# Kernel optimization log

Hardware: AMD Instinct MI355X
Metric: run time of the kernel (lower is better)

## Reference

```python
import jax, jax.numpy as jnp
import numpy as np

P = 16            # decode steps == n_process
M = 4             # number of physical nodes
CAPACITY = [4, 4, 4, 4]
B = 4096          # batch
S = 16            # n_process (sequence length)
G = 128           # gnn_dim
E = 256           # n_embed
H = 512           # n_hidden
CLIP = 10.0       # clip_logits
MASK_PENALTY = 1e8


def setup_inputs() -> dict:
    key = jax.random.key(0)
    ks = jax.random.split(key, 16)
    u = lambda k, shape: jax.random.uniform(k, shape, jnp.float32, -0.08, 0.08)
    return {
        "x": jax.random.normal(ks[0], (B, S, G), jnp.float32),
        "emb_W": u(ks[1], (E, G)),                 # embedding Linear (no bias)
        "enc_Wih": u(ks[2], (4 * H, E)),           # encoder LSTM (gate order i,f,g,o)
        "enc_Whh": u(ks[3], (4 * H, H)),
        "enc_b": u(ks[4], (4 * H,)),               # b_ih + b_hh folded into one bias
        "dec_Wih": u(ks[5], (4 * H, E)),           # decoder LSTM
        "dec_Whh": u(ks[6], (4 * H, H)),
        "dec_b": u(ks[7], (4 * H,)),
        "Wq2": u(ks[8], (H, H)),                   # pointer W_q2
        "bq2": u(ks[9], (H,)),
        "Wref2": u(ks[10], (H, H)),                # pointer W_ref2 (conv1d k=1 == linear)
        "bref2": u(ks[11], (H,)),
        "Vec2": u(ks[12], (H,)),
        "dec_input0": u(ks[13], (E,)),             # learned initial decoder input
    }


def lstm_cell(x, h, c, Wih, Whh, b):
    g = x @ Wih.T + h @ Whh.T + b
    i, f, gg, o = jnp.split(g, 4, axis=-1)
    c = jax.nn.sigmoid(f) * c + jax.nn.sigmoid(i) * jnp.tanh(gg)
    h = jax.nn.sigmoid(o) * jnp.tanh(c)
    return h, c


def reference(x, emb_W, enc_Wih, enc_Whh, enc_b, dec_Wih, dec_Whh, dec_b,
              Wq2, bq2, Wref2, bref2, Vec2, dec_input0):
    Bx, Sx, _ = x.shape
    emb = x @ emb_W.T                                  # (B,S,E)

    # ---- encoder LSTM over the sequence ----
    def enc_step(carry, xt):
        h, c = carry
        h, c = lstm_cell(xt, h, c, enc_Wih, enc_Whh, enc_b)
        return (h, c), h

    h0 = jnp.zeros((Bx, H), emb.dtype)
    (h, c), enc_hs = jax.lax.scan(enc_step, (h0, h0), jnp.swapaxes(emb, 0, 1))
    ref = jnp.swapaxes(enc_hs, 0, 1)                   # (B,S,H)

    # W_ref2 conv1d(k=1) applied to ref is step-invariant: hoist out of the loop
    u2 = jnp.einsum('bsh,oh->bso', ref, Wref2) + bref2  # (B,S,H)

    dec0 = jnp.broadcast_to(dec_input0, (Bx, E))
    mask0 = jnp.zeros((Bx, Sx), emb.dtype)

    def dec_step(carry, _):
        h, c, din, mask = carry
        h, c = lstm_cell(din, h, c, dec_Wih, dec_Whh, dec_b)
        qp = h @ Wq2.T + bq2                           # (B,H)
        t = CLIP * jnp.tanh(qp[:, None, :] + u2)       # (B,S,H)
        logits = jnp.einsum('h,bsh->bs', Vec2, t) - MASK_PENALTY * mask
        log_p = jax.nn.log_softmax(logits, axis=-1)    # (B,S)
        nxt = jnp.argmax(log_p, axis=1)                # greedy node selector
        din = jnp.take_along_axis(emb, nxt[:, None, None], axis=1)[:, 0, :]
        mask = mask + jax.nn.one_hot(nxt, Sx, dtype=mask.dtype)
        return (h, c, din, mask), (nxt, log_p)

    _, (pis, log_ps) = jax.lax.scan(dec_step, (h, c, dec0, mask0), None, length=P)
    pi = jnp.swapaxes(pis, 0, 1)                       # (B,P)
    log_ps = jnp.swapaxes(log_ps, 0, 1)                # (B,P,S)

    # log-likelihood of the chosen tour
    ll = jnp.take_along_axis(log_ps, pi[:, :, None], axis=2)[..., 0].sum(axis=1)

    # __get_mapping: node id per step depends only on the capacity vector
    nodes = jnp.asarray(np.repeat(np.arange(M), np.asarray(CAPACITY))[:P], jnp.int32)
    rows = jnp.arange(Bx)
    mapping = jnp.full((Bx, P), -1, jnp.int32)
    mapping = mapping.at[rows[:, None], pi].set(jnp.broadcast_to(nodes, (Bx, P)))
    return mapping, ll
```

## Files before the change

### kernel.cpp

```cpp
#include <hip/hip_runtime.h>
#include <cstddef>

#define Bsz  4096
#define Sseq 16
#define Gdim 128
#define Edim 256
#define Hdim 512
#define H4   2048
#define Psteps 16
#define BK   16

typedef short bfrag8 __attribute__((ext_vector_type(8)));
typedef float f32x4  __attribute__((ext_vector_type(4)));

__device__ __forceinline__ void split3(float f, unsigned short& h,
                                       unsigned short& m, unsigned short& l) {
    unsigned u = __float_as_uint(f);
    h = (unsigned short)(u >> 16);
    float r1 = f - __uint_as_float(u & 0xffff0000u);
    unsigned u1 = __float_as_uint(r1);
    m = (unsigned short)(u1 >> 16);
    float r2 = r1 - __uint_as_float(u1 & 0xffff0000u);
    l = (unsigned short)(__float_as_uint(r2) >> 16);
}

__global__ void fold_kernel(const float* __restrict__ encWih,
                            const float* __restrict__ encWhh,
                            const float* __restrict__ enc_b,
                            const float* __restrict__ decWih,
                            const float* __restrict__ decWhh,
                            const float* __restrict__ dec_b,
                            const float* __restrict__ embW,
                            const float* __restrict__ dec0,
                            unsigned short* __restrict__ encEh,
                            unsigned short* __restrict__ encEm,
                            unsigned short* __restrict__ encEl,
                            unsigned short* __restrict__ encWh,
                            unsigned short* __restrict__ encWm,
                            unsigned short* __restrict__ encWl,
                            unsigned short* __restrict__ decEh,
                            unsigned short* __restrict__ decEm,
                            unsigned short* __restrict__ decEl,
                            unsigned short* __restrict__ decWh,
                            unsigned short* __restrict__ decWm,
                            unsigned short* __restrict__ decWl,
                            float* __restrict__ encBI, float* __restrict__ decBI,
                            float* __restrict__ v0bI) {
    const int o = blockIdx.x;
    const int gate = o >> 9, j = o & 511;
    const int c = j * 4 + gate;
    const int g = threadIdx.x;
    float se = 0.f, sd = 0.f;
    for (int e = 0; e < Edim; ++e) {
        float w = embW[e * Gdim + g];
        se += encWih[(size_t)o * Edim + e] * w;
        sd += decWih[(size_t)o * Edim + e] * w;
    }
    unsigned short h, m, l;
    split3(se, h, m, l);
    encEh[(size_t)c * Gdim + g] = h; encEm[(size_t)c * Gdim + g] = m;
    encEl[(size_t)c * Gdim + g] = l;
    split3(sd, h, m, l);
    decEh[(size_t)c * Gdim + g] = h; decEm[(size_t)c * Gdim + g] = m;
    decEl[(size_t)c * Gdim + g] = l;
    for (int k = g; k < Hdim; k += Gdim) {
        split3(encWhh[(size_t)o * Hdim + k], h, m, l);
        encWh[(size_t)c * Hdim + k] = h; encWm[(size_t)c * Hdim + k] = m;
        encWl[(size_t)c * Hdim + k] = l;
        split3(decWhh[(size_t)o * Hdim + k], h, m, l);
        decWh[(size_t)c * Hdim + k] = h; decWm[(size_t)c * Hdim + k] = m;
        decWl[(size_t)c * Hdim + k] = l;
    }
    if (g == 0) {
        encBI[c] = enc_b[o];
        decBI[c] = dec_b[o];
        float s = dec_b[o];
        for (int e = 0; e < Edim; ++e) s += decWih[(size_t)o * Edim + e] * dec0[e];
        v0bI[c] = s;
    }
}

__global__ __launch_bounds__(256) void gates_mfma(
    const unsigned short* __restrict__ Wh1, const unsigned short* __restrict__ Wm1,
    const unsigned short* __restrict__ Wl1, int K1,
    const float* __restrict__ X, int ldx,
    const int* __restrict__ gather, int gmul,
    const unsigned short* __restrict__ Wh2, const unsigned short* __restrict__ Wm2,
    const unsigned short* __restrict__ Wl2, int K2,
    const float* __restrict__ Hin,
    const float* __restrict__ biasI,
    const float* __restrict__ c_in, float* __restrict__ h_out,
    float* __restrict__ c_out, int czero)
{
    __shared__ __align__(16) unsigned short wlds[2][3 * 4096];
    __shared__ __align__(16) float alds[2][128 * 32];

    const int tid = threadIdx.x;
    const int wv = tid >> 6, lane = tid & 63;
    const int lm = lane & 15, quad = lane >> 4;
    const int c0 = blockIdx.y * 128;
    const int mB0 = blockIdx.x * 128;

    int mrow[2];
#pragma unroll
    for (int tm = 0; tm < 2; ++tm) mrow[tm] = mB0 + wv * 32 + tm * 16 + lm;

    int srow[2], sqs[2];
#pragma unroll
    for (int i = 0; i < 2; ++i) {
        const int seg = i * 4 + wv;
        const int r = seg * 16 + (lane >> 2);
        srow[i] = r;
        sqs[i] = (lane & 3) ^ ((r >> 1) & 3);
    }
    size_t roff1[2], roff2[2];
#pragma unroll
    for (int i = 0; i < 2; ++i) {
        roff1[i] = (size_t)(c0 + srow[i]) * K1 + (size_t)(sqs[i] * 8);
        roff2[i] = (size_t)(c0 + srow[i]) * K2 + (size_t)(sqs[i] * 8);
    }

    const int asw = ((lane & 7) ^ (lane >> 3)) * 4;
    const float* asrcX[4];
    const float* asrcH[4];
#pragma unroll
    for (int i = 0; i < 4; ++i) {
        const int r = (wv * 4 + i) * 8 + (lane >> 3);
        const int m = mB0 + r;
        if (X) {
            size_t off = (size_t)m * ldx;
            if (gather) off += (size_t)gather[m] * gmul;
            asrcX[i] = X + off + asw;
        }
        if (Hin) asrcH[i] = Hin + (size_t)m * K2 + asw;
    }

    int boffW[8];
#pragma unroll
    for (int tn = 0; tn < 8; ++tn) {
        const int r = tn * 16 + lm;
        boffW[tn] = r * 32 + ((quad ^ ((r >> 1) & 3)) * 8);
    }
    int boffA1[2], boffA2[2];
#pragma unroll
    for (int tm = 0; tm < 2; ++tm) {
        const int r = wv * 32 + tm * 16 + lm;
        boffA1[tm] = r * 32 + (((2 * quad)     ^ (lm & 7)) << 2);
        boffA2[tm] = r * 32 + (((2 * quad + 1) ^ (lm & 7)) << 2);
    }

    auto stage = [&](int kcN, int buf) {
        const bool nX = kcN < K1;
        const int kb = nX ? kcN : kcN - K1;
#pragma unroll
        for (int i = 0; i < 2; ++i) {
            const int seg = i * 4 + wv;
            unsigned short* lb = &wlds[buf][seg * 512];
            const unsigned short* gh = (nX ? Wh1 + roff1[i] : Wh2 + roff2[i]) + kb;
            const unsigned short* gm = (nX ? Wm1 + roff1[i] : Wm2 + roff2[i]) + kb;
            const unsigned short* gl = (nX ? Wl1 + roff1[i] : Wl2 + roff2[i]) + kb;
            __builtin_amdgcn_global_load_lds(
                (const __attribute__((address_space(1))) void*)gh,
                (__attribute__((address_space(3))) void*)(lb), 16, 0, 0);
            __builtin_amdgcn_global_load_lds(
                (const __attribute__((address_space(1))) void*)gm,
                (__attribute__((address_space(3))) void*)(lb + 4096), 16, 0, 0);
            __builtin_amdgcn_global_load_lds(
                (const __attribute__((address_space(1))) void*)gl,
                (__attribute__((address_space(3))) void*)(lb + 8192), 16, 0, 0);
        }
#pragma unroll
        for (int i = 0; i < 4; ++i) {
            float* lb = &alds[buf][(wv * 4 + i) * 256];
            const float* src = (nX ? asrcX[i] : asrcH[i]) + kb;
            __builtin_amdgcn_global_load_lds(
                (const __attribute__((address_space(1))) void*)src,
                (__attribute__((address_space(3))) void*)lb, 16, 0, 0);
        }
    };

    f32x4 acc[8][2];
#pragma unroll
    for (int i = 0; i < 8; ++i)
#pragma unroll
        for (int j = 0; j < 2; ++j) acc[i][j] = (f32x4){0.f, 0.f, 0.f, 0.f};

    const int KT = K1 + K2;
    stage(0, 0);
    int cur = 0;

    for (int kc = 0; kc < KT; kc += 32) {
        __syncthreads();
        if (kc + 32 < KT) stage(kc + 32, cur ^ 1);

        const float* abuf = alds[cur];
        bfrag8 bh[2], bm[2], bl[2];
#pragma unroll
        for (int tm = 0; tm < 2; ++tm) {
            float a8[8];
            *(float4*)&a8[0] = *(const float4*)(abuf + boffA1[tm]);
            *(float4*)&a8[4] = *(const float4*)(abuf + boffA2[tm]);
#pragma unroll
            for (int j = 0; j < 8; ++j) {
                unsigned short h, m, l;
                split3(a8[j], h, m, l);
                bh[tm][j] = (short)h; bm[tm][j] = (short)m; bl[tm][j] = (short)l;
            }
        }

        const unsigned short* bufp = wlds[cur];
#pragma unroll
        for (int hh = 0; hh < 2; ++hh) {
            bfrag8 ah[4], am4[4], al[4];
#pragma unroll
            for (int t = 0; t < 4; ++t) {
                const int tn = hh * 4 + t;
                ah[t]  = *(const bfrag8*)(bufp + boffW[tn]);
                am4[t] = *(const bfrag8*)(bufp + 4096 + boffW[tn]);
                al[t]  = *(const bfrag8*)(bufp + 8192 + boffW[tn]);
            }
#pragma unroll
            for (int tm = 0; tm < 2; ++tm) {
#pragma unroll
                for (int t = 0; t < 4; ++t) {
                    const int tn = hh * 4 + t;
                    f32x4 c = acc[tn][tm];
                    c = __builtin_amdgcn_mfma_f32_16x16x32_bf16(ah[t], bl[tm], c, 0, 0, 0);
                    c = __builtin_amdgcn_mfma_f32_16x16x32_bf16(al[t], bh[tm], c, 0, 0, 0);
                    c = __builtin_amdgcn_mfma_f32_16x16x32_bf16(am4[t], bm[tm], c, 0, 0, 0);
                    c = __builtin_amdgcn_mfma_f32_16x16x32_bf16(ah[t], bm[tm], c, 0, 0, 0);
                    c = __builtin_amdgcn_mfma_f32_16x16x32_bf16(am4[t], bh[tm], c, 0, 0, 0);
                    c = __builtin_amdgcn_mfma_f32_16x16x32_bf16(ah[t], bh[tm], c, 0, 0, 0);
                    acc[tn][tm] = c;
                }
            }
        }
        cur ^= 1;
    }

#pragma unroll
    for (int tn = 0; tn < 8; ++tn) {
        const int nb = c0 + tn * 16 + quad * 4;
        float4 bb = *(const float4*)(biasI + nb);
        const int j = nb >> 2;
#pragma unroll
        for (int tm = 0; tm < 2; ++tm) {
            const size_t idx = (size_t)mrow[tm] * Hdim + j;
            float gi = acc[tn][tm][0] + bb.x;
            float gf = acc[tn][tm][1] + bb.y;
            float gg = acc[tn][tm][2] + bb.z;
            float go = acc[tn][tm][3] + bb.w;
            float si = 1.f / (1.f + expf(-gi));
            float sf = 1.f / (1.f + expf(-gf));
            float so = 1.f / (1.f + expf(-go));
            float co = czero ? 0.f : c_in[idx];
            float cn = si * tanhf(gg) + sf * co;
            c_out[idx] = cn;
            h_out[idx] = so * tanhf(cn);
        }
    }
}

__global__ __launch_bounds__(256, 4) void gemm_sm(const float* __restrict__ A,
                                                  const float* __restrict__ W,
                                                  const float* __restrict__ bias,
                                                  float* __restrict__ C, int ldc)
{
    __shared__ float As[BK][64];
    __shared__ float Bs[BK][64];
    const int tid = threadIdx.x;
    const int rowBase = blockIdx.y * 64;
    const int colBase = blockIdx.x * 64;
    const int wv = tid >> 6;
    const int waveX = wv & 1, waveY = wv >> 1;
    const int lane = tid & 63;
    const int lx = lane & 7, ly = lane >> 3;
    const int rOff = waveY * 32 + ly * 4;
    const int cOff = waveX * 32 + lx * 4;

    const int ra = tid & 63;
    const int ka = (tid >> 6) * 4;
    const float* arow = A + (size_t)(rowBase + ra) * Hdim + ka;
    const float* brow = W + (size_t)(colBase + ra) * Hdim + ka;

    float4 aR, bR;
    float acc[4][4];
#pragma unroll
    for (int i = 0; i < 4; ++i)
#pragma unroll
        for (int j = 0; j < 4; ++j) acc[i][j] = 0.f;

    aR = *(const float4*)(arow);
    bR = *(const float4*)(brow);
    for (int kt = 0; kt < Hdim; kt += BK) {
        __syncthreads();
        As[ka + 0][ra] = aR.x; As[ka + 1][ra] = aR.y;
        As[ka + 2][ra] = aR.z; As[ka + 3][ra] = aR.w;
        Bs[ka + 0][ra] = bR.x; Bs[ka + 1][ra] = bR.y;
        Bs[ka + 2][ra] = bR.z; Bs[ka + 3][ra] = bR.w;
        __syncthreads();
        if (kt + BK < Hdim) {
            aR = *(const float4*)(arow + kt + BK);
            bR = *(const float4*)(brow + kt + BK);
        }
#pragma unroll
        for (int kk = 0; kk < BK; ++kk) {
            float4 av = *(const float4*)&As[kk][rOff];
            float4 bv = *(const float4*)&Bs[kk][cOff];
            const float* ap = (const float*)&av;
            const float* bp = (const float*)&bv;
#pragma unroll
            for (int i = 0; i < 4; ++i)
#pragma unroll
                for (int j = 0; j < 4; ++j) acc[i][j] += ap[i] * bp[j];
        }
    }

    float4 bb = *(const float4*)(bias + colBase + cOff);
#pragma unroll
    for (int i = 0; i < 4; ++i) {
        const int row = rowBase + rOff + i;
        float4 o;
        o.x = acc[i][0] + bb.x;
        o.y = acc[i][1] + bb.y;
        o.z = acc[i][2] + bb.z;
        o.w = acc[i][3] + bb.w;
        *(float4*)(C + (size_t)row * ldc + colBase + cOff) = o;
    }
}

__global__ __launch_bounds__(256) void attn_step(const float* __restrict__ qp,
                                                 const float* __restrict__ u2,
                                                 const float* __restrict__ Vec2,
                                                 float* __restrict__ mask,
                                                 float* __restrict__ ll_ws,
                                                 int* __restrict__ nxt,
                                                 float* __restrict__ out_map,
                                                 float* __restrict__ out_ll,
                                                 int step, int node) {
    const int b = blockIdx.x;
    __shared__ float qpS[Hdim];
    __shared__ float vS[Hdim];
    __shared__ float logitS[Sseq];
    const int tid = threadIdx.x;
    qpS[tid]       = qp[(size_t)b * Hdim + tid];
    qpS[tid + 256] = qp[(size_t)b * Hdim + 256 + tid];
    vS[tid]        = Vec2[tid];
    vS[tid + 256]  = Vec2[256 + tid];
    __syncthreads();

    const int wave = tid >> 6, lane = tid & 63;
    for (int si = 0; si < 4; ++si) {
        int s = wave * 4 + si;
        const float* u2p = u2 + ((size_t)b * Sseq + s) * Hdim;
        float sum = 0.f;
#pragma unroll
        for (int i = 0; i < 8; ++i) {
            int hh = lane + i * 64;
            sum += vS[hh] * tanhf(qpS[hh] + u2p[hh]);
        }
        for (int off = 32; off > 0; off >>= 1) sum += __shfl_down(sum, off);
        if (lane == 0) {
            float pen = step ? mask[b * Sseq + s] * 1e8f : 0.f;
            logitS[s] = 10.f * sum - pen;
        }
    }
    __syncthreads();

    if (tid == 0) {
        float mx = logitS[0];
        int am = 0;
        for (int s = 1; s < Sseq; ++s)
            if (logitS[s] > mx) { mx = logitS[s]; am = s; }
        float se = 0.f;
        for (int s = 0; s < Sseq; ++s) se += expf(logitS[s] - mx);
        float lp = -logf(se);
        float llv = (step ? ll_ws[b] : 0.f) + lp;
        ll_ws[b] = llv;
        out_ll[b] = llv;
        nxt[b] = am;
        if (step == 0) {
            for (int s = 0; s < Sseq; ++s) mask[b * Sseq + s] = (s == am) ? 1.f : 0.f;
        } else {
            mask[b * Sseq + am] += 1.f;
        }
        out_map[b * Sseq + am] = (float)node;
    }
}

extern "C" void kernel_launch(void* const* d_in, const int* in_sizes, int n_in,
                              void* d_out, int out_size, void* d_ws, size_t ws_size,
                              hipStream_t stream) {
    const float* x       = (const float*)d_in[0];
    const float* emb_W   = (const float*)d_in[1];
    const float* enc_Wih = (const float*)d_in[2];
    const float* enc_Whh = (const float*)d_in[3];
    const float* enc_b   = (const float*)d_in[4];
    const float* dec_Wih = (const float*)d_in[5];
    const float* dec_Whh = (const float*)d_in[6];
    const float* dec_b   = (const float*)d_in[7];
    const float* Wq2     = (const float*)d_in[8];
    const float* bq2     = (const float*)d_in[9];
    const float* Wref2   = (const float*)d_in[10];
    const float* bref2   = (const float*)d_in[11];
    const float* Vec2    = (const float*)d_in[12];
    const float* dec0    = (const float*)d_in[13];

    float* ws      = (float*)d_ws;
    float* u2      = ws;
    float* h0      = u2 + (size_t)Bsz * Sseq * Hdim;
    float* c0      = h0 + (size_t)Bsz * Hdim;
    float* h1      = c0 + (size_t)Bsz * Hdim;
    float* c1      = h1 + (size_t)Bsz * Hdim;
    float* qp      = c1 + (size_t)Bsz * Hdim;
    float* mask    = qp + (size_t)Bsz * Hdim;
    float* ll      = mask + (size_t)Bsz * Sseq;
    int*   nxt     = (int*)(ll + Bsz);
    float* encBI   = (float*)(nxt + Bsz);
    float* decBI   = encBI + H4;
    float* v0bI    = decBI + H4;
    unsigned short* us = (unsigned short*)(v0bI + H4);
    unsigned short* encEh = us;                       us += (size_t)H4 * Gdim;
    unsigned short* encEm = us;                       us += (size_t)H4 * Gdim;
    unsigned short* encEl = us;                       us += (size_t)H4 * Gdim;
    unsigned short* encWh = us;                       us += (size_t)H4 * Hdim;
    unsigned short* encWm = us;                       us += (size_t)H4 * Hdim;
    unsigned short* encWl = us;                       us += (size_t)H4 * Hdim;
    unsigned short* decEh = us;                       us += (size_t)H4 * Gdim;
    unsigned short* decEm = us;                       us += (size_t)H4 * Gdim;
    unsigned short* decEl = us;                       us += (size_t)H4 * Gdim;
    unsigned short* decWh = us;                       us += (size_t)H4 * Hdim;
    unsigned short* decWm = us;                       us += (size_t)H4 * Hdim;
    unsigned short* decWl = us;                       us += (size_t)H4 * Hdim;

    float* out_map = (float*)d_out;
    float* out_ll  = out_map + (size_t)Bsz * Psteps;

    static const int nodes[Psteps] = {0,0,0,0, 1,1,1,1, 2,2,2,2, 3,3,3,3};

    fold_kernel<<<H4, Gdim, 0, stream>>>(enc_Wih, enc_Whh, enc_b,
                                         dec_Wih, dec_Whh, dec_b,
                                         emb_W, dec0,
                                         encEh, encEm, encEl, encWh, encWm, encWl,
                                         decEh, decEm, decEl, decWh, decWm, decWl,
                                         encBI, decBI, v0bI);

    const dim3 gBig(32, 16);
    const dim3 gSm(8, 64);

    for (int t = 0; t < Sseq; ++t) {
        float* ho = (t & 1) ? h0 : h1;
        float* co = (t & 1) ? c0 : c1;
        const float* hi = (t & 1) ? h1 : h0;
        const float* ci = (t & 1) ? c1 : c0;
        if (t == 0) {
            gates_mfma<<<gBig, 256, 0, stream>>>(
                encEh, encEm, encEl, Gdim,
                x, Sseq * Gdim, nullptr, 0,
                nullptr, nullptr, nullptr, 0, nullptr,
                encBI, ci, ho, co, 1);
        } else {
            gates_mfma<<<gBig, 256, 0, stream>>>(
                encEh, encEm, encEl, Gdim,
                x + t * Gdim, Sseq * Gdim, nullptr, 0,
                encWh, encWm, encWl, Hdim, hi,
                encBI, ci, ho, co, 0);
        }
        gemm_sm<<<gSm, 256, 0, stream>>>(ho, Wref2, bref2,
                                         u2 + (size_t)t * Hdim, Sseq * Hdim);
    }

    for (int p = 0; p < Psteps; ++p) {
        const int u = Sseq + p;
        float* ho = (u & 1) ? h0 : h1;
        float* co = (u & 1) ? c0 : c1;
        const float* hi = (u & 1) ? h1 : h0;
        const float* ci = (u & 1) ? c1 : c0;
        if (p == 0) {
            gates_mfma<<<gBig, 256, 0, stream>>>(
                nullptr, nullptr, nullptr, 0,
                nullptr, 0, nullptr, 0,
                decWh, decWm, decWl, Hdim, hi,
                v0bI, ci, ho, co, 0);
        } else {
            gates_mfma<<<gBig, 256, 0, stream>>>(
                decEh, decEm, decEl, Gdim,
                x, Sseq * Gdim, nxt, Gdim,
                decWh, decWm, decWl, Hdim, hi,
                decBI, ci, ho, co, 0);
        }
        gemm_sm<<<gSm, 256, 0, stream>>>(ho, Wq2, bq2, qp, Hdim);
        attn_step<<<Bsz, 256, 0, stream>>>(qp, u2, Vec2, mask, ll, nxt,
                                           out_map, out_ll, p, nodes[p]);
    }
}
```

Baseline: 3.862 ms.

## Replace FP32 SIMT projection GEMMs with split-bf16 MFMA kernels

The W_ref2 and W_q2 projections, run once per encoder and decoder step, move from a scalar FP32 tiled GEMM to an MFMA kernel. It splits weights and activations into three bf16 parts and runs six cross-product MFMAs to keep close to FP32 accuracy. Weights are pre-split once by a new fold kernel and staged into LDS with double-buffered direct global-to-LDS loads and swizzled layouts. The fold kernel also caches the Wih rows in shared memory instead of re-reading them from global memory. The cost is extra workspace, a small one-time setup pass, and accuracy that depends on the three-way split.

Result: faster. 3.252 ms (-15.8%).

```diff
diff --git a/kernel.cpp b/kernel.cpp
--- a/kernel.cpp
+++ b/kernel.cpp
@@ -46,15 +46,23 @@
                             unsigned short* __restrict__ decWl,
                             float* __restrict__ encBI, float* __restrict__ decBI,
                             float* __restrict__ v0bI) {
+    __shared__ float rE[Edim], rD[Edim];
     const int o = blockIdx.x;
     const int gate = o >> 9, j = o & 511;
     const int c = j * 4 + gate;
     const int g = threadIdx.x;
+    rE[g]        = encWih[(size_t)o * Edim + g];
+    rE[g + Gdim] = encWih[(size_t)o * Edim + g + Gdim];
+    rD[g]        = decWih[(size_t)o * Edim + g];
+    rD[g + Gdim] = decWih[(size_t)o * Edim + g + Gdim];
+    __syncthreads();
+
     float se = 0.f, sd = 0.f;
+#pragma unroll 8
     for (int e = 0; e < Edim; ++e) {
         float w = embW[e * Gdim + g];
-        se += encWih[(size_t)o * Edim + e] * w;
-        sd += decWih[(size_t)o * Edim + e] * w;
+        se += rE[e] * w;
+        sd += rD[e] * w;
     }
     unsigned short h, m, l;
     split3(se, h, m, l);
@@ -75,8 +83,28 @@
         encBI[c] = enc_b[o];
         decBI[c] = dec_b[o];
         float s = dec_b[o];
-        for (int e = 0; e < Edim; ++e) s += decWih[(size_t)o * Edim + e] * dec0[e];
+        for (int e = 0; e < Edim; ++e) s += rD[e] * dec0[e];
         v0bI[c] = s;
+    }
+}
+
+__global__ __launch_bounds__(256) void fold_proj(
+    const float* __restrict__ Wr, const float* __restrict__ Wq,
+    unsigned short* __restrict__ rWh, unsigned short* __restrict__ rWm,
+    unsigned short* __restrict__ rWl,
+    unsigned short* __restrict__ qWh, unsigned short* __restrict__ qWm,
+    unsigned short* __restrict__ qWl) {
+    const int o = blockIdx.x;
+    const float* src = blockIdx.y ? Wq : Wr;
+    unsigned short* ph = blockIdx.y ? qWh : rWh;
+    unsigned short* pm = blockIdx.y ? qWm : rWm;
+    unsigned short* pl = blockIdx.y ? qWl : rWl;
+    for (int k = threadIdx.x; k < Hdim; k += 256) {
+        unsigned short h, m, l;
+        split3(src[(size_t)o * Hdim + k], h, m, l);
+        ph[(size_t)o * Hdim + k] = h;
+        pm[(size_t)o * Hdim + k] = m;
+        pl[(size_t)o * Hdim + k] = l;
     }
 }
 
@@ -261,71 +289,116 @@
     }
 }
 
-__global__ __launch_bounds__(256, 4) void gemm_sm(const float* __restrict__ A,
-                                                  const float* __restrict__ W,
-                                                  const float* __restrict__ bias,
-                                                  float* __restrict__ C, int ldc)
+__global__ __launch_bounds__(256) void proj_mfma(
+    const unsigned short* __restrict__ Wh, const unsigned short* __restrict__ Wm,
+    const unsigned short* __restrict__ Wl,
+    const float* __restrict__ A,
+    const float* __restrict__ bias,
+    float* __restrict__ C, int ldc)
 {
-    __shared__ float As[BK][64];
-    __shared__ float Bs[BK][64];
+    __shared__ __align__(16) unsigned short wlds[2][3 * 2048];
+    __shared__ __align__(16) float alds[2][64 * 32];
+
     const int tid = threadIdx.x;
-    const int rowBase = blockIdx.y * 64;
-    const int colBase = blockIdx.x * 64;
-    const int wv = tid >> 6;
-    const int waveX = wv & 1, waveY = wv >> 1;
-    const int lane = tid & 63;
-    const int lx = lane & 7, ly = lane >> 3;
-    const int rOff = waveY * 32 + ly * 4;
-    const int cOff = waveX * 32 + lx * 4;
-
-    const int ra = tid & 63;
-    const int ka = (tid >> 6) * 4;
-    const float* arow = A + (size_t)(rowBase + ra) * Hdim + ka;
-    const float* brow = W + (size_t)(colBase + ra) * Hdim + ka;
-
-    float4 aR, bR;
-    float acc[4][4];
-#pragma unroll
-    for (int i = 0; i < 4; ++i)
-#pragma unroll
-        for (int j = 0; j < 4; ++j) acc[i][j] = 0.f;
-
-    aR = *(const float4*)(arow);
-    bR = *(const float4*)(brow);
-    for (int kt = 0; kt < Hdim; kt += BK) {
+    const int wv = tid >> 6, lane = tid & 63;
+    const int lm = lane & 15, quad = lane >> 4;
+    const int nB0 = blockIdx.y * 64;
+    const int mB0 = blockIdx.x * 64;
+
+    const int rw = tid >> 2;
+    const int sqw = (tid & 3) ^ ((rw >> 1) & 3);
+    const size_t wroff = (size_t)(nB0 + rw) * Hdim + (size_t)(sqw * 8);
+
+    const int asw = ((lane & 7) ^ (lane >> 3)) * 4;
+    const float* asrc[2];
+#pragma unroll
+    for (int i = 0; i < 2; ++i) {
+        const int r = i * 32 + wv * 8 + (lane >> 3);
+        asrc[i] = A + (size_t)(mB0 + r) * Hdim + asw;
+    }
+
+    int boffW[4];
+#pragma unroll
+    for (int tn = 0; tn < 4; ++tn) {
+        const int r = tn * 16 + lm;
+        boffW[tn] = r * 32 + ((quad ^ ((r >> 1) & 3)) * 8);
+    }
+    const int ra = wv * 16 + lm;
+    const int boffA1 = ra * 32 + (((2 * quad)     ^ (lm & 7)) << 2);
+    const int boffA2 = ra * 32 + (((2 * quad + 1) ^ (lm & 7)) << 2);
+
+    auto stage = [&](int kb, int buf) {
+        unsigned short* lb0 = &wlds[buf][wv * 512];
+        __builtin_amdgcn_global_load_lds(
+            (const __attribute__((address_space(1))) void*)(Wh + wroff + kb),
+            (__attribute__((address_space(3))) void*)(lb0), 16, 0, 0);
+        __builtin_amdgcn_global_load_lds(
+            (const __attribute__((address_space(1))) void*)(Wm + wroff + kb),
+            (__attribute__((address_space(3))) void*)(lb0 + 2048), 16, 0, 0);
+        __builtin_amdgcn_global_load_lds(
+            (const __attribute__((address_space(1))) void*)(Wl + wroff + kb),
+            (__attribute__((address_space(3))) void*)(lb0 + 4096), 16, 0, 0);
+#pragma unroll
+        for (int i = 0; i < 2; ++i) {
+            float* lb = &alds[buf][(i * 32 + wv * 8) * 32];
+            __builtin_amdgcn_global_load_lds(
+                (const __attribute__((address_space(1))) void*)(asrc[i] + kb),
+                (__attribute__((address_space(3))) void*)lb, 16, 0, 0);
+        }
+    };
+
+    f32x4 acc[4];
+#pragma unroll
+    for (int i = 0; i < 4; ++i) acc[i] = (f32x4){0.f, 0.f, 0.f, 0.f};
+
+    stage(0, 0);
+    int cur = 0;
+
+    for (int kc = 0; kc < Hdim; kc += 32) {
         __syncthreads();
-        As[ka + 0][ra] = aR.x; As[ka + 1][ra] = aR.y;
-        As[ka + 2][ra] = aR.z; As[ka + 3][ra] = aR.w;
-        Bs[ka + 0][ra] = bR.x; Bs[ka + 1][ra] = bR.y;
-        Bs[ka + 2][ra] = bR.z; Bs[ka + 3][ra] = bR.w;
-        __syncthreads();
-        if (kt + BK < Hdim) {
-            aR = *(const float4*)(arow + kt + BK);
-            bR = *(const float4*)(brow + kt + BK);
-        }
-#pragma unroll
-        for (int kk = 0; kk < BK; ++kk) {
-            float4 av = *(const float4*)&As[kk][rOff];
-            float4 bv = *(const float4*)&Bs[kk][cOff];
-            const float* ap = (const float*)&av;
-            const float* bp = (const float*)&bv;
-#pragma unroll
-            for (int i = 0; i < 4; ++i)
-#pragma unroll
-                for (int j = 0; j < 4; ++j) acc[i][j] += ap[i] * bp[j];
-        }
-    }
-
-    float4 bb = *(const float4*)(bias + colBase + cOff);
-#pragma unroll
-    for (int i = 0; i < 4; ++i) {
-        const int row = rowBase + rOff + i;
+        if (kc + 32 < Hdim) stage(kc + 32, cur ^ 1);
+
+        const float* abuf = alds[cur];
+        float a8[8];
+        *(float4*)&a8[0] = *(const float4*)(abuf + boffA1);
+        *(float4*)&a8[4] = *(const float4*)(abuf + boffA2);
+        bfrag8 bh, bm, bl;
+#pragma unroll
+        for (int j = 0; j < 8; ++j) {
+            unsigned short h, m, l;
+            split3(a8[j], h, m, l);
+            bh[j] = (short)h; bm[j] = (short)m; bl[j] = (short)l;
+        }
+
+        const unsigned short* bufp = wlds[cur];
+#pragma unroll
+        for (int tn = 0; tn < 4; ++tn) {
+            bfrag8 ah  = *(const bfrag8*)(bufp + boffW[tn]);
+            bfrag8 am4 = *(const bfrag8*)(bufp + 2048 + boffW[tn]);
+            bfrag8 al  = *(const bfrag8*)(bufp + 4096 + boffW[tn]);
+            f32x4 c = acc[tn];
+            c = __builtin_amdgcn_mfma_f32_16x16x32_bf16(ah,  bl, c, 0, 0, 0);
+            c = __builtin_amdgcn_mfma_f32_16x16x32_bf16(al,  bh, c, 0, 0, 0);
+            c = __builtin_amdgcn_mfma_f32_16x16x32_bf16(am4, bm, c, 0, 0, 0);
+            c = __builtin_amdgcn_mfma_f32_16x16x32_bf16(ah,  bm, c, 0, 0, 0);
+            c = __builtin_amdgcn_mfma_f32_16x16x32_bf16(am4, bh, c, 0, 0, 0);
+            c = __builtin_amdgcn_mfma_f32_16x16x32_bf16(ah,  bh, c, 0, 0, 0);
+            acc[tn] = c;
+        }
+        cur ^= 1;
+    }
+
+    const int m = mB0 + wv * 16 + lm;
+#pragma unroll
+    for (int tn = 0; tn < 4; ++tn) {
+        const int n = nB0 + tn * 16 + quad * 4;
+        float4 bb = *(const float4*)(bias + n);
         float4 o;
-        o.x = acc[i][0] + bb.x;
-        o.y = acc[i][1] + bb.y;
-        o.z = acc[i][2] + bb.z;
-        o.w = acc[i][3] + bb.w;
-        *(float4*)(C + (size_t)row * ldc + colBase + cOff) = o;
+        o.x = acc[tn][0] + bb.x;
+        o.y = acc[tn][1] + bb.y;
+        o.z = acc[tn][2] + bb.z;
+        o.w = acc[tn][3] + bb.w;
+        *(float4*)(C + (size_t)m * ldc + n) = o;
     }
 }
 
@@ -432,6 +505,12 @@
     unsigned short* decWh = us;                       us += (size_t)H4 * Hdim;
     unsigned short* decWm = us;                       us += (size_t)H4 * Hdim;
     unsigned short* decWl = us;                       us += (size_t)H4 * Hdim;
+    unsigned short* prWh = us;                        us += (size_t)Hdim * Hdim;
+    unsigned short* prWm = us;                        us += (size_t)Hdim * Hdim;
+    unsigned short* prWl = us;                        us += (size_t)Hdim * Hdim;
+    unsigned short* pqWh = us;                        us += (size_t)Hdim * Hdim;
+    unsigned short* pqWm = us;                        us += (size_t)Hdim * Hdim;
+    unsigned short* pqWl = us;                        us += (size_t)Hdim * Hdim;
 
     float* out_map = (float*)d_out;
     float* out_ll  = out_map + (size_t)Bsz * Psteps;
@@ -444,9 +523,12 @@
                                          encEh, encEm, encEl, encWh, encWm, encWl,
                                          decEh, decEm, decEl, decWh, decWm, decWl,
                                          encBI, decBI, v0bI);
+    fold_proj<<<dim3(Hdim, 2), 256, 0, stream>>>(Wref2, Wq2,
+                                                 prWh, prWm, prWl,
+                                                 pqWh, pqWm, pqWl);
 
     const dim3 gBig(32, 16);
-    const dim3 gSm(8, 64);
+    const dim3 gPr(64, 8);
 
     for (int t = 0; t < Sseq; ++t) {
         float* ho = (t & 1) ? h0 : h1;
@@ -466,8 +548,8 @@
                 encWh, encWm, encWl, Hdim, hi,
                 encBI, ci, ho, co, 0);
         }
-        gemm_sm<<<gSm, 256, 0, stream>>>(ho, Wref2, bref2,
-                                         u2 + (size_t)t * Hdim, Sseq * Hdim);
+        proj_mfma<<<gPr, 256, 0, stream>>>(prWh, prWm, prWl, ho, bref2,
+                                           u2 + (size_t)t * Hdim, Sseq * Hdim);
     }
 
     for (int p = 0; p < Psteps; ++p) {
@@ -489,7 +571,8 @@
                 decWh, decWm, decWl, Hdim, hi,
                 decBI, ci, ho, co, 0);
         }
-        gemm_sm<<<gSm, 256, 0, stream>>>(ho, Wq2, bq2, qp, Hdim);
+        proj_mfma<<<gPr, 256, 0, stream>>>(pqWh, pqWm, pqWl, ho, bq2,
+                                           qp, Hdim);
         attn_step<<<Bsz, 256, 0, stream>>>(qp, u2, Vec2, mask, ll, nxt,
                                            out_map, out_ll, p, nodes[p]);
     }
```
